# Kernel optimization log

Measured on AMD Instinct MI355X. Metric: run time of the kernel, lower is better.

## Reference

```python
import jax, jax.numpy as jnp
import numpy as np

N_NODES = 100000
N_EDGES = 1600000
N_GRAPHS = 256
BN_EPS = 1e-5


def _graph_conv(x, src, dst, ew, w_rel, b_rel, w_root):
    # PyG GraphConv: aggregate add of edge_weight * x[src] at dst, then dense transform
    msg = x[src] * ew[:, None]                      # [E, F] gathered messages
    agg = jax.ops.segment_sum(msg, dst, num_segments=N_NODES)  # [N, F]
    return agg @ w_rel + b_rel + x @ w_root


def _bn_eval(x, g, b, m, v):
    return (x - m) * jax.lax.rsqrt(v + BN_EPS) * g + b


def setup_inputs() -> dict:
    key = jax.random.key(0)
    ks = jax.random.split(key, 32)
    d = {}
    d["x"] = jax.random.normal(ks[0], (N_NODES, 29), dtype=jnp.float32)
    d["edge_index"] = jax.random.randint(ks[1], (2, N_EDGES), 0, N_NODES, dtype=jnp.int64)
    d["edge_weight"] = jax.random.uniform(ks[2], (N_EDGES,), dtype=jnp.float32)
    d["batch"] = jnp.sort(jax.random.randint(ks[3], (N_NODES,), 0, N_GRAPHS, dtype=jnp.int64))
    dims = [(29, 256), (256, 128), (128, 64), (64, 32)]
    for i, (fi, fo) in enumerate(dims, start=1):
        s = 1.0 / np.sqrt(fi)
        d[f"w{i}_rel"] = jax.random.uniform(ks[4 + 3 * i], (fi, fo), minval=-s, maxval=s, dtype=jnp.float32)
        d[f"b{i}_rel"] = jax.random.uniform(ks[5 + 3 * i], (fo,), minval=-s, maxval=s, dtype=jnp.float32)
        d[f"w{i}_root"] = jax.random.uniform(ks[6 + 3 * i], (fi, fo), minval=-s, maxval=s, dtype=jnp.float32)
    for j, c in enumerate([128, 64, 32], start=1):
        kb = jax.random.split(jax.random.fold_in(key, 100 + j), 4)
        d[f"bn{j}_g"] = 1.0 + 0.1 * jax.random.normal(kb[0], (c,), dtype=jnp.float32)
        d[f"bn{j}_b"] = 0.1 * jax.random.normal(kb[1], (c,), dtype=jnp.float32)
        d[f"bn{j}_m"] = 0.1 * jax.random.normal(kb[2], (c,), dtype=jnp.float32)
        d[f"bn{j}_v"] = 0.5 + jax.random.uniform(kb[3], (c,), dtype=jnp.float32)
    s = 1.0 / np.sqrt(32.0)
    d["fc_w"] = jax.random.uniform(ks[30], (32, 1), minval=-s, maxval=s, dtype=jnp.float32)
    d["fc_b"] = jax.random.uniform(ks[31], (1,), minval=-s, maxval=s, dtype=jnp.float32)
    return d


def reference(x, edge_index, edge_weight, batch,
              w1_rel, b1_rel, w1_root, w2_rel, b2_rel, w2_root,
              w3_rel, b3_rel, w3_root, w4_rel, b4_rel, w4_root,
              bn1_g, bn1_b, bn1_m, bn1_v,
              bn2_g, bn2_b, bn2_m, bn2_v,
              bn3_g, bn3_b, bn3_m, bn3_v,
              fc_w, fc_b):
    src, dst = edge_index[0], edge_index[1]
    h = jax.nn.relu(_graph_conv(x, src, dst, edge_weight, w1_rel, b1_rel, w1_root))
    h = _graph_conv(h, src, dst, edge_weight, w2_rel, b2_rel, w2_root)
    h = jax.nn.relu(_bn_eval(h, bn1_g, bn1_b, bn1_m, bn1_v))
    h = _graph_conv(h, src, dst, edge_weight, w3_rel, b3_rel, w3_root)
    h = jax.nn.relu(_bn_eval(h, bn2_g, bn2_b, bn2_m, bn2_v))
    h = _graph_conv(h, src, dst, edge_weight, w4_rel, b4_rel, w4_root)
    h = jax.nn.relu(_bn_eval(h, bn3_g, bn3_b, bn3_m, bn3_v))
    # global mean pool over graphs
    sums = jax.ops.segment_sum(h, batch, num_segments=N_GRAPHS)        # [G, 32]
    cnts = jax.ops.segment_sum(jnp.ones((h.shape[0],), h.dtype), batch, num_segments=N_GRAPHS)
    pooled = sums / jnp.maximum(cnts, 1.0)[:, None]
    return jax.nn.sigmoid(pooled @ fc_w + fc_b)                         # [G, 1]
```

## Files before the change

### kernel.cpp

```cpp
#include <hip/hip_runtime.h>
#include <math.h>

#define N_NODES 100000
#define N_EDGES 1600000
#define N_GRAPHS 256
#define BN_EPS 1e-5f

__global__ void hist_kernel(const int* __restrict__ ei, int* __restrict__ deg) {
    int e = blockIdx.x * blockDim.x + threadIdx.x;
    if (e < N_EDGES) atomicAdd(&deg[ei[N_EDGES + e]], 1);
}

__global__ void scan1_kernel(const int* __restrict__ deg, int* __restrict__ rowptr,
                             int* __restrict__ bsum) {
    __shared__ int s[256];
    int tid = threadIdx.x;
    int i = blockIdx.x * 256 + tid;
    int v = (i < N_NODES) ? deg[i] : 0;
    s[tid] = v; __syncthreads();
    for (int off = 1; off < 256; off <<= 1) {
        int t = (tid >= off) ? s[tid - off] : 0; __syncthreads();
        s[tid] += t; __syncthreads();
    }
    if (i < N_NODES) rowptr[i] = s[tid] - v;
    if (tid == 255) bsum[blockIdx.x] = s[255];
}

__global__ void scan2_kernel(int* bsum, int nb) {
    __shared__ int s[512];
    int tid = threadIdx.x;
    int v = (tid < nb) ? bsum[tid] : 0;
    s[tid] = v; __syncthreads();
    for (int off = 1; off < 512; off <<= 1) {
        int t = (tid >= off) ? s[tid - off] : 0; __syncthreads();
        s[tid] += t; __syncthreads();
    }
    if (tid < nb) bsum[tid] = s[tid] - v;
}

__global__ void scan3_kernel(int* __restrict__ rowptr, const int* __restrict__ bsum) {
    int i = blockIdx.x * 256 + threadIdx.x;
    if (i < N_NODES) rowptr[i] += bsum[blockIdx.x];
    if (i == 0) rowptr[N_NODES] = N_EDGES;
}

__global__ void scatter_kernel(const int* __restrict__ ei, const float* __restrict__ ew,
                               const int* __restrict__ rowptr, int* __restrict__ cnt,
                               int* __restrict__ ssrc, float* __restrict__ swt) {
    int e = blockIdx.x * blockDim.x + threadIdx.x;
    if (e >= N_EDGES) return;
    int dst = ei[N_EDGES + e];
    int pos = rowptr[dst] + atomicAdd(&cnt[dst], 1);
    ssrc[pos] = ei[e];
    swt[pos] = ew[e];
}

__global__ void bnprep_kernel(const float* __restrict__ v1, const float* __restrict__ v2,
                              const float* __restrict__ v3, float* __restrict__ rs) {
    int t = threadIdx.x;
    if (t < 128) rs[t] = 1.0f / sqrtf(v1[t] + BN_EPS);
    if (t < 64)  rs[128 + t] = 1.0f / sqrtf(v2[t] + BN_EPS);
    if (t < 32)  rs[192 + t] = 1.0f / sqrtf(v3[t] + BN_EPS);
}

__global__ void starts_kernel(const int* __restrict__ batch, int* __restrict__ starts) {
    int i = blockIdx.x * 256 + threadIdx.x;
    if (i >= N_NODES) return;
    int b = batch[i];
    int bp = (i == 0) ? -1 : batch[i - 1];
    for (int g = bp + 1; g <= b; ++g) starts[g] = i;
    if (i == N_NODES - 1)
        for (int g = b + 1; g <= N_GRAPHS; ++g) starts[g] = N_NODES;
}

__global__ __launch_bounds__(256) void pad_x_kernel(const float* __restrict__ x,
                                                    float* __restrict__ xp) {
    int i = blockIdx.x * 256 + threadIdx.x;
    if (i >= N_NODES * 32) return;
    int n = i >> 5, c = i & 31;
    xp[i] = (c < 29) ? x[n * 29 + c] : 0.f;
}

__global__ __launch_bounds__(256) void agg_x_kernel(const float* __restrict__ xp,
        const int* __restrict__ rowptr, const int* __restrict__ ssrc,
        const float* __restrict__ swt, float* __restrict__ agg) {
    int tid = threadIdx.x;
    int node = blockIdx.x * 32 + (tid >> 3);
    int c = (tid & 7) * 4;
    int e0 = rowptr[node], e1 = rowptr[node + 1];
    float4 acc = {0.f, 0.f, 0.f, 0.f};
    int e = e0;
    for (; e < e1 && (e & 3); ++e) {
        int s0 = ssrc[e]; float w0 = swt[e];
        float4 y0 = *(const float4*)&xp[(size_t)s0 * 32 + c];
        acc.x = fmaf(w0, y0.x, acc.x); acc.y = fmaf(w0, y0.y, acc.y);
        acc.z = fmaf(w0, y0.z, acc.z); acc.w = fmaf(w0, y0.w, acc.w);
    }
    for (; e + 4 <= e1; e += 4) {
        int4   s4 = *(const int4*)&ssrc[e];
        float4 w4 = *(const float4*)&swt[e];
        float4 y0 = *(const float4*)&xp[(size_t)s4.x * 32 + c];
        float4 y1 = *(const float4*)&xp[(size_t)s4.y * 32 + c];
        float4 y2 = *(const float4*)&xp[(size_t)s4.z * 32 + c];
        float4 y3 = *(const float4*)&xp[(size_t)s4.w * 32 + c];
        acc.x = fmaf(w4.x, y0.x, acc.x); acc.y = fmaf(w4.x, y0.y, acc.y);
        acc.z = fmaf(w4.x, y0.z, acc.z); acc.w = fmaf(w4.x, y0.w, acc.w);
        acc.x = fmaf(w4.y, y1.x, acc.x); acc.y = fmaf(w4.y, y1.y, acc.y);
        acc.z = fmaf(w4.y, y1.z, acc.z); acc.w = fmaf(w4.y, y1.w, acc.w);
        acc.x = fmaf(w4.z, y2.x, acc.x); acc.y = fmaf(w4.z, y2.y, acc.y);
        acc.z = fmaf(w4.z, y2.z, acc.z); acc.w = fmaf(w4.z, y2.w, acc.w);
        acc.x = fmaf(w4.w, y3.x, acc.x); acc.y = fmaf(w4.w, y3.y, acc.y);
        acc.z = fmaf(w4.w, y3.z, acc.z); acc.w = fmaf(w4.w, y3.w, acc.w);
    }
    for (; e < e1; ++e) {
        int s0 = ssrc[e]; float w0 = swt[e];
        float4 y0 = *(const float4*)&xp[(size_t)s0 * 32 + c];
        acc.x = fmaf(w0, y0.x, acc.x); acc.y = fmaf(w0, y0.y, acc.y);
        acc.z = fmaf(w0, y0.z, acc.z); acc.w = fmaf(w0, y0.w, acc.w);
    }
    *(float4*)&agg[(size_t)node * 32 + c] = acc;
}

__global__ __launch_bounds__(256) void dense1_kernel(const float* __restrict__ agg,
        const float* __restrict__ xp, const float* __restrict__ wrel,
        const float* __restrict__ wroot, const float* __restrict__ bias,
        float* __restrict__ out) {
    __shared__ float sA[32 * 32];
    __shared__ float sX[32 * 32];
    int tid = threadIdx.x;
    int node0 = blockIdx.x * 32;
    ((float4*)sA)[tid] = ((const float4*)(agg + (size_t)node0 * 32))[tid];
    ((float4*)sX)[tid] = ((const float4*)(xp + (size_t)node0 * 32))[tid];
    __syncthreads();
    int ct = tid & 63;
    int mg = tid >> 6;
    int c0 = ct * 4;
    float acc[8][4];
#pragma unroll
    for (int m = 0; m < 8; m++)
#pragma unroll
        for (int j = 0; j < 4; j++) acc[m][j] = 0.f;
    for (int k = 0; k < 29; k++) {
        float4 wr = *(const float4*)&wrel[k * 256 + c0];
        float4 wo = *(const float4*)&wroot[k * 256 + c0];
#pragma unroll
        for (int m = 0; m < 8; m++) {
            float sa = sA[(mg * 8 + m) * 32 + k];
            float sx = sX[(mg * 8 + m) * 32 + k];
            acc[m][0] = fmaf(sa, wr.x, fmaf(sx, wo.x, acc[m][0]));
            acc[m][1] = fmaf(sa, wr.y, fmaf(sx, wo.y, acc[m][1]));
            acc[m][2] = fmaf(sa, wr.z, fmaf(sx, wo.z, acc[m][2]));
            acc[m][3] = fmaf(sa, wr.w, fmaf(sx, wo.w, acc[m][3]));
        }
    }
    float4 b4 = *(const float4*)&bias[c0];
#pragma unroll
    for (int m = 0; m < 8; m++) {
        int row = node0 + mg * 8 + m;
        float4 o;
        o.x = fmaxf(acc[m][0] + b4.x, 0.f);
        o.y = fmaxf(acc[m][1] + b4.y, 0.f);
        o.z = fmaxf(acc[m][2] + b4.z, 0.f);
        o.w = fmaxf(acc[m][3] + b4.w, 0.f);
        *(float4*)&out[(size_t)row * 256 + c0] = o;
    }
}

template <int K, int F, int RPM, int KC>
__global__ __launch_bounds__(256) void gemm_dual_kernel(const float* __restrict__ in,
        const float* __restrict__ wA, const float* __restrict__ wB,
        float* __restrict__ outA, float* __restrict__ outB) {
    constexpr int NT = 256;
    constexpr int NCT = F / 2;
    constexpr int MG = NT / NCT;
    constexpr int ROWS = MG * RPM;
    constexpr int KC4 = KC / 4;
    __shared__ float s[ROWS * KC];
    int tid = threadIdx.x;
    size_t node0 = (size_t)blockIdx.x * ROWS;
    int ct = tid % NCT;
    int mg = tid / NCT;
    int c0 = ct * 4;
    const float* W;
    float* OUT;
    int cc;
    if (c0 < F) { W = wA; OUT = outA; cc = c0; }
    else        { W = wB; OUT = outB; cc = c0 - F; }
    float acc[RPM][4];
#pragma unroll
    for (int m = 0; m < RPM; m++)
#pragma unroll
        for (int j = 0; j < 4; j++) acc[m][j] = 0.f;
    const float* srow = s + (size_t)(mg * RPM) * KC;
    for (int kb = 0; kb < K; kb += KC) {
        __syncthreads();
        for (int idx = tid; idx < ROWS * KC4; idx += NT) {
            int rr = idx / KC4;
            int c4 = idx % KC4;
            *(float4*)&s[rr * KC + c4 * 4] =
                *(const float4*)&in[(node0 + rr) * K + kb + c4 * 4];
        }
        __syncthreads();
        for (int k0 = 0; k0 < KC; k0 += 4) {
            float4 w0 = *(const float4*)&W[(kb + k0 + 0) * F + cc];
            float4 w1 = *(const float4*)&W[(kb + k0 + 1) * F + cc];
            float4 w2 = *(const float4*)&W[(kb + k0 + 2) * F + cc];
            float4 w3 = *(const float4*)&W[(kb + k0 + 3) * F + cc];
#pragma unroll
            for (int m = 0; m < RPM; m++) {
                float4 sm = *(const float4*)&srow[m * KC + k0];
                acc[m][0] = fmaf(sm.x, w0.x, acc[m][0]);
                acc[m][1] = fmaf(sm.x, w0.y, acc[m][1]);
                acc[m][2] = fmaf(sm.x, w0.z, acc[m][2]);
                acc[m][3] = fmaf(sm.x, w0.w, acc[m][3]);
                acc[m][0] = fmaf(sm.y, w1.x, acc[m][0]);
                acc[m][1] = fmaf(sm.y, w1.y, acc[m][1]);
                acc[m][2] = fmaf(sm.y, w1.z, acc[m][2]);
                acc[m][3] = fmaf(sm.y, w1.w, acc[m][3]);
                acc[m][0] = fmaf(sm.z, w2.x, acc[m][0]);
                acc[m][1] = fmaf(sm.z, w2.y, acc[m][1]);
                acc[m][2] = fmaf(sm.z, w2.z, acc[m][2]);
                acc[m][3] = fmaf(sm.z, w2.w, acc[m][3]);
                acc[m][0] = fmaf(sm.w, w3.x, acc[m][0]);
                acc[m][1] = fmaf(sm.w, w3.y, acc[m][1]);
                acc[m][2] = fmaf(sm.w, w3.z, acc[m][2]);
                acc[m][3] = fmaf(sm.w, w3.w, acc[m][3]);
            }
        }
    }
#pragma unroll
    for (int m = 0; m < RPM; m++) {
        size_t row = node0 + mg * RPM + m;
        float4 o = {acc[m][0], acc[m][1], acc[m][2], acc[m][3]};
        *(float4*)&OUT[row * F + cc] = o;
    }
}

template <int F>
__global__ __launch_bounds__(256) void combine_kernel(const float* __restrict__ y,
        const float* __restrict__ r, const int* __restrict__ rowptr,
        const int* __restrict__ ssrc, const float* __restrict__ swt,
        const float* __restrict__ bias, const float* __restrict__ bg,
        const float* __restrict__ bb, const float* __restrict__ bm,
        const float* __restrict__ rs, float* __restrict__ h) {
    constexpr int TPN = F / 4;
    int tid = threadIdx.x;
    int node = blockIdx.x * (256 / TPN) + tid / TPN;
    int c = (tid % TPN) * 4;
    int e0 = rowptr[node], e1 = rowptr[node + 1];
    float4 acc = {0.f, 0.f, 0.f, 0.f};
    int e = e0;
    for (; e < e1 && (e & 3); ++e) {
        int s0 = ssrc[e]; float w0 = swt[e];
        float4 y0 = *(const float4*)&y[(size_t)s0 * F + c];
        acc.x = fmaf(w0, y0.x, acc.x); acc.y = fmaf(w0, y0.y, acc.y);
        acc.z = fmaf(w0, y0.z, acc.z); acc.w = fmaf(w0, y0.w, acc.w);
    }
    for (; e + 4 <= e1; e += 4) {
        int4   s4 = *(const int4*)&ssrc[e];
        float4 w4 = *(const float4*)&swt[e];
        float4 y0 = *(const float4*)&y[(size_t)s4.x * F + c];
        float4 y1 = *(const float4*)&y[(size_t)s4.y * F + c];
        float4 y2 = *(const float4*)&y[(size_t)s4.z * F + c];
        float4 y3 = *(const float4*)&y[(size_t)s4.w * F + c];
        acc.x = fmaf(w4.x, y0.x, acc.x); acc.y = fmaf(w4.x, y0.y, acc.y);
        acc.z = fmaf(w4.x, y0.z, acc.z); acc.w = fmaf(w4.x, y0.w, acc.w);
        acc.x = fmaf(w4.y, y1.x, acc.x); acc.y = fmaf(w4.y, y1.y, acc.y);
        acc.z = fmaf(w4.y, y1.z, acc.z); acc.w = fmaf(w4.y, y1.w, acc.w);
        acc.x = fmaf(w4.z, y2.x, acc.x); acc.y = fmaf(w4.z, y2.y, acc.y);
        acc.z = fmaf(w4.z, y2.z, acc.z); acc.w = fmaf(w4.z, y2.w, acc.w);
        acc.x = fmaf(w4.w, y3.x, acc.x); acc.y = fmaf(w4.w, y3.y, acc.y);
        acc.z = fmaf(w4.w, y3.z, acc.z); acc.w = fmaf(w4.w, y3.w, acc.w);
    }
    for (; e < e1; ++e) {
        int s0 = ssrc[e]; float w0 = swt[e];
        float4 y0 = *(const float4*)&y[(size_t)s0 * F + c];
        acc.x = fmaf(w0, y0.x, acc.x); acc.y = fmaf(w0, y0.y, acc.y);
        acc.z = fmaf(w0, y0.z, acc.z); acc.w = fmaf(w0, y0.w, acc.w);
    }
    float4 bi = *(const float4*)&bias[c];
    float4 rv = *(const float4*)&r[(size_t)node * F + c];
    float4 mu = *(const float4*)&bm[c];
    float4 rq = *(const float4*)&rs[c];
    float4 gm = *(const float4*)&bg[c];
    float4 bt = *(const float4*)&bb[c];
    float4 o;
    o.x = fmaxf((acc.x + bi.x + rv.x - mu.x) * rq.x * gm.x + bt.x, 0.f);
    o.y = fmaxf((acc.y + bi.y + rv.y - mu.y) * rq.y * gm.y + bt.y, 0.f);
    o.z = fmaxf((acc.z + bi.z + rv.z - mu.z) * rq.z * gm.z + bt.z, 0.f);
    o.w = fmaxf((acc.w + bi.w + rv.w - mu.w) * rq.w * gm.w + bt.w, 0.f);
    *(float4*)&h[(size_t)node * F + c] = o;
}

__global__ __launch_bounds__(256) void pool_fc_kernel(const float* __restrict__ h4,
        const int* __restrict__ starts, const float* __restrict__ fcw,
        const float* __restrict__ fcb, float* __restrict__ out) {
    int g = blockIdx.x;
    int tid = threadIdx.x;
    int i0 = starts[g], i1 = starts[g + 1];
    int ch = tid & 31, part = tid >> 5;
    float sum = 0.f;
    for (int i = i0 + part; i < i1; i += 8) sum += h4[(size_t)i * 32 + ch];
    __shared__ float sm[8][32];
    sm[part][ch] = sum;
    __syncthreads();
    if (tid < 32) {
        float tot = 0.f;
        for (int p = 0; p < 8; p++) tot += sm[p][tid];
        float cnt = (float)(i1 - i0);
        float mean = tot / fmaxf(cnt, 1.0f);
        sm[0][tid] = mean * fcw[tid];
    }
    __syncthreads();
    if (tid == 0) {
        float z = 0.f;
        for (int c = 0; c < 32; c++) z += sm[0][c];
        z += fcb[0];
        out[g] = 1.0f / (1.0f + expf(-z));
    }
}

extern "C" void kernel_launch(void* const* d_in, const int* in_sizes, int n_in,
                              void* d_out, int out_size, void* d_ws, size_t ws_size,
                              hipStream_t stream) {
    (void)in_sizes; (void)n_in; (void)out_size; (void)ws_size;
    const float* x       = (const float*)d_in[0];
    const int*   ei      = (const int*)d_in[1];
    const float* ew      = (const float*)d_in[2];
    const int*   batch   = (const int*)d_in[3];
    const float* w1_rel  = (const float*)d_in[4];
    const float* b1      = (const float*)d_in[5];
    const float* w1_root = (const float*)d_in[6];
    const float* w2_rel  = (const float*)d_in[7];
    const float* b2      = (const float*)d_in[8];
    const float* w2_root = (const float*)d_in[9];
    const float* w3_rel  = (const float*)d_in[10];
    const float* b3      = (const float*)d_in[11];
    const float* w3_root = (const float*)d_in[12];
    const float* w4_rel  = (const float*)d_in[13];
    const float* b4      = (const float*)d_in[14];
    const float* w4_root = (const float*)d_in[15];
    const float* bn1_g = (const float*)d_in[16];
    const float* bn1_b = (const float*)d_in[17];
    const float* bn1_m = (const float*)d_in[18];
    const float* bn2_g = (const float*)d_in[20];
    const float* bn2_b = (const float*)d_in[21];
    const float* bn2_m = (const float*)d_in[22];
    const float* bn3_g = (const float*)d_in[24];
    const float* bn3_b = (const float*)d_in[25];
    const float* bn3_m = (const float*)d_in[26];
    const float* fc_w = (const float*)d_in[28];
    const float* fc_b = (const float*)d_in[29];

    char* ws = (char*)d_ws;
    int*   rowptr = (int*)(ws + 0);
    int*   cnt    = (int*)(ws + (1ull << 20));
    int*   bsum   = (int*)(ws + (2ull << 20));
    float* rs     = (float*)(ws + (2ull << 20) + (64ull << 10));
    int*   starts = (int*)(ws + (2ull << 20) + (128ull << 10));
    int*   ssrc   = (int*)(ws + (4ull << 20));
    float* swt    = (float*)(ws + (11ull << 20));
    float* bufA   = (float*)(ws + (18ull << 20));
    float* bufB   = (float*)(ws + (122ull << 20));
    float* bufC   = (float*)(ws + (174ull << 20));
    float* xp   = bufB;
    float* agg1 = bufC;

    hipMemsetAsync(cnt, 0, N_NODES * 4, stream);
    hist_kernel<<<6250, 256, 0, stream>>>(ei, cnt);
    scan1_kernel<<<391, 256, 0, stream>>>(cnt, rowptr, bsum);
    scan2_kernel<<<1, 512, 0, stream>>>(bsum, 391);
    scan3_kernel<<<391, 256, 0, stream>>>(rowptr, bsum);
    hipMemsetAsync(cnt, 0, N_NODES * 4, stream);
    scatter_kernel<<<6250, 256, 0, stream>>>(ei, ew, rowptr, cnt, ssrc, swt);
    bnprep_kernel<<<1, 128, 0, stream>>>((const float*)d_in[19], (const float*)d_in[23],
                                         (const float*)d_in[27], rs);
    starts_kernel<<<391, 256, 0, stream>>>(batch, starts);

    pad_x_kernel<<<12500, 256, 0, stream>>>(x, xp);
    agg_x_kernel<<<3125, 256, 0, stream>>>(xp, rowptr, ssrc, swt, agg1);
    dense1_kernel<<<3125, 256, 0, stream>>>(agg1, xp, w1_rel, w1_root, b1, bufA);

    gemm_dual_kernel<256, 128, 16, 64><<<1563, 256, 0, stream>>>(bufA, w2_rel, w2_root, bufB, bufC);
    combine_kernel<128><<<12500, 256, 0, stream>>>(bufB, bufC, rowptr, ssrc, swt,
                                                   b2, bn1_g, bn1_b, bn1_m, rs, bufC);

    gemm_dual_kernel<128, 64, 8, 64><<<1563, 256, 0, stream>>>(bufC, w3_rel, w3_root, bufB, bufA);
    combine_kernel<64><<<6250, 256, 0, stream>>>(bufB, bufA, rowptr, ssrc, swt,
                                                 b3, bn2_g, bn2_b, bn2_m, rs + 128, bufA);

    gemm_dual_kernel<64, 32, 8, 32><<<782, 256, 0, stream>>>(bufA, w4_rel, w4_root, bufB, bufC);
    combine_kernel<32><<<3125, 256, 0, stream>>>(bufB, bufC, rowptr, ssrc, swt,
                                                 b4, bn3_g, bn3_b, bn3_m, rs + 192, bufC);

    pool_fc_kernel<<<N_GRAPHS, 256, 0, stream>>>(bufC, starts, fc_w, fc_b, (float*)d_out);
}
```

Measured before the change: 773.6 us.

## Fuse layer-1 dense transform into layer-2 dual GEMM via shared-memory tiles

Replaces the separate layer-1 dense kernel and layer-2 dual GEMM with one kernel. Each 64-node block computes the ReLU'd 256-wide layer-1 activations in 64-column chunks into shared memory, then consumes each chunk immediately in the layer-2 rel/root GEMM. This removes the global write and re-read of the 100000x256 intermediate activation tensor and one launch. In exchange it adds register pressure and per-chunk synchronisation, and the layer-1 weight loads are serialized inside the block.

```diff
diff --git a/kernel.cpp b/kernel.cpp
--- a/kernel.cpp
+++ b/kernel.cpp
@@ -121,48 +121,105 @@
     *(float4*)&agg[(size_t)node * 32 + c] = acc;
 }
 
-__global__ __launch_bounds__(256) void dense1_kernel(const float* __restrict__ agg,
-        const float* __restrict__ xp, const float* __restrict__ wrel,
-        const float* __restrict__ wroot, const float* __restrict__ bias,
-        float* __restrict__ out) {
-    __shared__ float sA[32 * 32];
-    __shared__ float sX[32 * 32];
-    int tid = threadIdx.x;
-    int node0 = blockIdx.x * 32;
-    ((float4*)sA)[tid] = ((const float4*)(agg + (size_t)node0 * 32))[tid];
-    ((float4*)sX)[tid] = ((const float4*)(xp + (size_t)node0 * 32))[tid];
+__global__ __launch_bounds__(256) void fused12_kernel(
+        const float* __restrict__ agg, const float* __restrict__ xp,
+        const float* __restrict__ w1r, const float* __restrict__ w1o,
+        const float* __restrict__ b1,
+        const float* __restrict__ w2A, const float* __restrict__ w2B,
+        float* __restrict__ outA, float* __restrict__ outB) {
+    constexpr int ROWS = 64, F2 = 128, K2 = 256, KC = 64;
+    __shared__ float sAgg[ROWS * 32];
+    __shared__ float sXp[ROWS * 32];
+    __shared__ float sH[ROWS * KC];
+    int tid = threadIdx.x;
+    size_t node0 = (size_t)blockIdx.x * ROWS;
+    {
+        const float4* ga = (const float4*)(agg + node0 * 32);
+        const float4* gx = (const float4*)(xp + node0 * 32);
+        ((float4*)sAgg)[tid]       = ga[tid];
+        ((float4*)sAgg)[tid + 256] = ga[tid + 256];
+        ((float4*)sXp)[tid]        = gx[tid];
+        ((float4*)sXp)[tid + 256]  = gx[tid + 256];
+    }
+    int cg = tid & 15, rg = tid >> 4;
+    int ct = tid & 63, mg = tid >> 6;
+    int c0 = ct * 4;
+    const float* W; float* OUT; int cc;
+    if (c0 < F2) { W = w2A; OUT = outA; cc = c0; }
+    else         { W = w2B; OUT = outB; cc = c0 - F2; }
+    float acc[16][4];
+#pragma unroll
+    for (int m = 0; m < 16; m++)
+#pragma unroll
+        for (int j = 0; j < 4; j++) acc[m][j] = 0.f;
     __syncthreads();
-    int ct = tid & 63;
-    int mg = tid >> 6;
-    int c0 = ct * 4;
-    float acc[8][4];
-#pragma unroll
-    for (int m = 0; m < 8; m++)
-#pragma unroll
-        for (int j = 0; j < 4; j++) acc[m][j] = 0.f;
-    for (int k = 0; k < 29; k++) {
-        float4 wr = *(const float4*)&wrel[k * 256 + c0];
-        float4 wo = *(const float4*)&wroot[k * 256 + c0];
-#pragma unroll
-        for (int m = 0; m < 8; m++) {
-            float sa = sA[(mg * 8 + m) * 32 + k];
-            float sx = sX[(mg * 8 + m) * 32 + k];
-            acc[m][0] = fmaf(sa, wr.x, fmaf(sx, wo.x, acc[m][0]));
-            acc[m][1] = fmaf(sa, wr.y, fmaf(sx, wo.y, acc[m][1]));
-            acc[m][2] = fmaf(sa, wr.z, fmaf(sx, wo.z, acc[m][2]));
-            acc[m][3] = fmaf(sa, wr.w, fmaf(sx, wo.w, acc[m][3]));
+#pragma unroll 1
+    for (int kb = 0; kb < K2; kb += KC) {
+        float accd[4][4];
+#pragma unroll
+        for (int rr = 0; rr < 4; rr++)
+#pragma unroll
+            for (int j = 0; j < 4; j++) accd[rr][j] = 0.f;
+        int dcol = kb + cg * 4;
+#pragma unroll 1
+        for (int k = 0; k < 29; k++) {
+            float4 wr = *(const float4*)&w1r[k * 256 + dcol];
+            float4 wo = *(const float4*)&w1o[k * 256 + dcol];
+#pragma unroll
+            for (int rr = 0; rr < 4; rr++) {
+                float sa = sAgg[(rg * 4 + rr) * 32 + k];
+                float sx = sXp[(rg * 4 + rr) * 32 + k];
+                accd[rr][0] = fmaf(sa, wr.x, fmaf(sx, wo.x, accd[rr][0]));
+                accd[rr][1] = fmaf(sa, wr.y, fmaf(sx, wo.y, accd[rr][1]));
+                accd[rr][2] = fmaf(sa, wr.z, fmaf(sx, wo.z, accd[rr][2]));
+                accd[rr][3] = fmaf(sa, wr.w, fmaf(sx, wo.w, accd[rr][3]));
+            }
         }
-    }
-    float4 b4 = *(const float4*)&bias[c0];
-#pragma unroll
-    for (int m = 0; m < 8; m++) {
-        int row = node0 + mg * 8 + m;
-        float4 o;
-        o.x = fmaxf(acc[m][0] + b4.x, 0.f);
-        o.y = fmaxf(acc[m][1] + b4.y, 0.f);
-        o.z = fmaxf(acc[m][2] + b4.z, 0.f);
-        o.w = fmaxf(acc[m][3] + b4.w, 0.f);
-        *(float4*)&out[(size_t)row * 256 + c0] = o;
+        float4 b4 = *(const float4*)&b1[dcol];
+#pragma unroll
+        for (int rr = 0; rr < 4; rr++) {
+            float4 o;
+            o.x = fmaxf(accd[rr][0] + b4.x, 0.f);
+            o.y = fmaxf(accd[rr][1] + b4.y, 0.f);
+            o.z = fmaxf(accd[rr][2] + b4.z, 0.f);
+            o.w = fmaxf(accd[rr][3] + b4.w, 0.f);
+            *(float4*)&sH[(rg * 4 + rr) * KC + cg * 4] = o;
+        }
+        __syncthreads();
+        const float* srow = sH + (size_t)(mg * 16) * KC;
+        for (int k0 = 0; k0 < KC; k0 += 4) {
+            float4 w0 = *(const float4*)&W[(kb + k0 + 0) * F2 + cc];
+            float4 w1 = *(const float4*)&W[(kb + k0 + 1) * F2 + cc];
+            float4 w2 = *(const float4*)&W[(kb + k0 + 2) * F2 + cc];
+            float4 w3 = *(const float4*)&W[(kb + k0 + 3) * F2 + cc];
+#pragma unroll
+            for (int m = 0; m < 16; m++) {
+                float4 sm = *(const float4*)&srow[m * KC + k0];
+                acc[m][0] = fmaf(sm.x, w0.x, acc[m][0]);
+                acc[m][1] = fmaf(sm.x, w0.y, acc[m][1]);
+                acc[m][2] = fmaf(sm.x, w0.z, acc[m][2]);
+                acc[m][3] = fmaf(sm.x, w0.w, acc[m][3]);
+                acc[m][0] = fmaf(sm.y, w1.x, acc[m][0]);
+                acc[m][1] = fmaf(sm.y, w1.y, acc[m][1]);
+                acc[m][2] = fmaf(sm.y, w1.z, acc[m][2]);
+                acc[m][3] = fmaf(sm.y, w1.w, acc[m][3]);
+                acc[m][0] = fmaf(sm.z, w2.x, acc[m][0]);
+                acc[m][1] = fmaf(sm.z, w2.y, acc[m][1]);
+                acc[m][2] = fmaf(sm.z, w2.z, acc[m][2]);
+                acc[m][3] = fmaf(sm.z, w2.w, acc[m][3]);
+                acc[m][0] = fmaf(sm.w, w3.x, acc[m][0]);
+                acc[m][1] = fmaf(sm.w, w3.y, acc[m][1]);
+                acc[m][2] = fmaf(sm.w, w3.z, acc[m][2]);
+                acc[m][3] = fmaf(sm.w, w3.w, acc[m][3]);
+            }
+        }
+        __syncthreads();
+    }
+#pragma unroll
+    for (int m = 0; m < 16; m++) {
+        size_t row = node0 + mg * 16 + m;
+        float4 o = {acc[m][0], acc[m][1], acc[m][2], acc[m][3]};
+        *(float4*)&OUT[row * F2 + cc] = o;
     }
 }
 
@@ -363,8 +420,8 @@
     float* bufA   = (float*)(ws + (18ull << 20));
     float* bufB   = (float*)(ws + (122ull << 20));
     float* bufC   = (float*)(ws + (174ull << 20));
-    float* xp   = bufB;
-    float* agg1 = bufC;
+    float* xp   = bufA;
+    float* agg1 = (float*)(ws + (32ull << 20));
 
     hipMemsetAsync(cnt, 0, N_NODES * 4, stream);
     hist_kernel<<<6250, 256, 0, stream>>>(ei, cnt);
@@ -379,9 +436,9 @@
 
     pad_x_kernel<<<12500, 256, 0, stream>>>(x, xp);
     agg_x_kernel<<<3125, 256, 0, stream>>>(xp, rowptr, ssrc, swt, agg1);
-    dense1_kernel<<<3125, 256, 0, stream>>>(agg1, xp, w1_rel, w1_root, b1, bufA);
-
-    gemm_dual_kernel<256, 128, 16, 64><<<1563, 256, 0, stream>>>(bufA, w2_rel, w2_root, bufB, bufC);
+
+    fused12_kernel<<<1563, 256, 0, stream>>>(agg1, xp, w1_rel, w1_root, b1,
+                                             w2_rel, w2_root, bufB, bufC);
     combine_kernel<128><<<12500, 256, 0, stream>>>(bufB, bufC, rowptr, ssrc, swt,
                                                    b2, bn1_g, bn1_b, bn1_m, rs, bufC);
 
```

New measurement: 788.7 us. About the same (+2.0%).
